# Optimization experiments

Measured on AMD Instinct MI355X. Metric: run time of the kernel, lower is better.

Reference implementation:

```python
import jax, jax.numpy as jnp
import numpy as np

B, N, D, H = 4, 2048, 1024, 16
HD = D // H


def setup_inputs() -> dict:
    key = jax.random.key(0)
    ks = jax.random.split(key, 9)
    s = 1.0 / np.sqrt(D)
    return {
        "x": jax.random.normal(ks[0], (B, N, D), jnp.float32),
        "Wq": jax.random.normal(ks[1], (D, D), jnp.float32) * s,
        "bq": jnp.zeros((D,), jnp.float32),
        "Wk": jax.random.normal(ks[2], (D, D), jnp.float32) * s,
        "bk": jnp.zeros((D,), jnp.float32),
        "Wv": jax.random.normal(ks[3], (D, D), jnp.float32) * s,
        "bv": jnp.zeros((D,), jnp.float32),
        "Wo": jax.random.normal(ks[4], (D, D), jnp.float32) * s,
        "bo": jnp.zeros((D,), jnp.float32),
    }


def reference(x, Wq, bq, Wk, bk, Wv, bv, Wo, bo):
    Bx, Nx, Dx = x.shape
    q = x @ Wq + bq  # [B,N,D]
    k = x @ Wk + bk
    v = x @ Wv + bv
    # split heads -> [B,H,N,hd]
    q = q.reshape(Bx, Nx, H, HD).transpose(0, 2, 1, 3)
    k = k.reshape(Bx, Nx, H, HD).transpose(0, 2, 1, 3)
    v = v.reshape(Bx, Nx, H, HD).transpose(0, 2, 1, 3)
    q = q / jnp.sqrt(jnp.asarray(HD, q.dtype))
    scores = jnp.einsum("bhqd,bhkd->bhqk", q, k)
    # causal mask: additive -1e9 strictly above diagonal (matches torch.triu diag=1)
    mask = jnp.triu(jnp.full((Nx, Nx), -1e9, dtype=scores.dtype), k=1)
    probs = jax.nn.softmax(scores + mask, axis=-1)
    out = jnp.einsum("bhqk,bhkd->bhqd", probs, v)  # [B,H,N,hd]
    out = out.transpose(0, 2, 1, 3).reshape(Bx, Nx, Dx)  # concat heads
    return out @ Wo + bo
```

## Files before the change

kernel.cpp:

```cpp
#include <hip/hip_runtime.h>
#include <hip/hip_bf16.h>


#define BB 4
#define NN 2048
#define DD 1024
#define HH 16
#define HD 64
#define MM (BB * NN)

typedef __bf16 bf16;
typedef __bf16 bf16x4 __attribute__((ext_vector_type(4)));
typedef __bf16 bf16x8 __attribute__((ext_vector_type(8)));
typedef float f32x4 __attribute__((ext_vector_type(4)));

__device__ __forceinline__ void async_copy16(bf16* lds, const bf16* g) {
    __builtin_amdgcn_global_load_lds(
        (const __attribute__((address_space(1))) void*)g,
        (__attribute__((address_space(3))) void*)lds, 16, 0, 0);
}

__global__ void convert_x(const float* __restrict__ x, bf16* __restrict__ xb) {
    int i = (blockIdx.x * 256 + threadIdx.x) * 4;
    float4 v = *(const float4*)&x[i];
    xb[i + 0] = (bf16)v.x;
    xb[i + 1] = (bf16)v.y;
    xb[i + 2] = (bf16)v.z;
    xb[i + 3] = (bf16)v.w;
}

__global__ void transpose_w4(const float* __restrict__ W0, const float* __restrict__ W1,
                             const float* __restrict__ W2, const float* __restrict__ W3,
                             bf16* __restrict__ Wt) {
    __shared__ float tile[32][33];
    const float* W = (blockIdx.z == 0) ? W0 : (blockIdx.z == 1) ? W1
                    : (blockIdx.z == 2) ? W2 : W3;
    bf16* out = Wt + (size_t)blockIdx.z * DD * DD;
    int tx = threadIdx.x, ty = threadIdx.y;
    int x0 = blockIdx.x * 32, y0 = blockIdx.y * 32;
#pragma unroll
    for (int i = 0; i < 32; i += 8)
        tile[ty + i][tx] = W[(size_t)(y0 + ty + i) * DD + x0 + tx];
    __syncthreads();
#pragma unroll
    for (int i = 0; i < 32; i += 8)
        out[(size_t)(x0 + ty + i) * DD + y0 + tx] = (bf16)tile[tx][ty + i];
}

template <int MODE>
__global__ __launch_bounds__(256) void gemm_bt(
    const bf16* __restrict__ A, const bf16* __restrict__ Wt,
    const float* __restrict__ b0, const float* __restrict__ b1,
    const float* __restrict__ b2, void* __restrict__ out0,
    void* __restrict__ out1, void* __restrict__ out2) {
    const int K = DD;
    __shared__ __align__(16) bf16 As[128 * 32];
    __shared__ __align__(16) bf16 Bs[128 * 32];
    __shared__ __align__(16) bf16 Cs[MODE == 0 ? 128 * 136 : 1];

    int m0 = blockIdx.x * 128;
    int n0 = blockIdx.y * 128;

    const bf16* Wz;
    const float* bias;
    void* out;
    float scale = 1.0f;
    int z = 0;
    if (MODE == 0) {
        z = blockIdx.z;
        Wz = Wt + (size_t)z * DD * DD;
        bias = (z == 0) ? b0 : ((z == 1) ? b1 : b2);
        out = (z == 0) ? out0 : ((z == 1) ? out1 : out2);
        if (z == 0) scale = 0.125f * 1.44269504f;
    } else {
        Wz = Wt; bias = b0; out = out0;
    }

    int tid = threadIdx.x;
    int w = tid >> 6, lane = tid & 63;
    int wm = w >> 1, wn = w & 1;
    int quad = lane >> 4, l16 = lane & 15;

    f32x4 acc[4][4];
#pragma unroll
    for (int i = 0; i < 4; i++)
#pragma unroll
        for (int j = 0; j < 4; j++) acc[i][j] = (f32x4){0.f, 0.f, 0.f, 0.f};

    for (int k0 = 0; k0 < K; k0 += 32) {
        __syncthreads();
#pragma unroll
        for (int j = 0; j < 2; j++) {
            int c = j * 256 + w * 64 + lane;
            int row = c >> 2, kk = (c & 3) * 8;
            async_copy16(&As[c * 8], &A[(size_t)(m0 + row) * K + k0 + kk]);
            async_copy16(&Bs[c * 8], &Wz[(size_t)(n0 + row) * K + k0 + kk]);
        }
        __syncthreads();

        bf16x8 af[4], bfm[4];
#pragma unroll
        for (int i = 0; i < 4; i++) {
            af[i] = *(const bf16x8*)&As[(wm * 64 + i * 16 + l16) * 32 + quad * 8];
            bfm[i] = *(const bf16x8*)&Bs[(wn * 64 + i * 16 + l16) * 32 + quad * 8];
        }
#pragma unroll
        for (int i = 0; i < 4; i++)
#pragma unroll
            for (int j = 0; j < 4; j++)
                acc[i][j] = __builtin_amdgcn_mfma_f32_16x16x32_bf16(
                    af[i], bfm[j], acc[i][j], 0, 0, 0);
    }

    if (MODE == 0) {
#pragma unroll
        for (int j = 0; j < 4; j++) {
            int nl = wn * 64 + j * 16 + l16;
            float bv = bias[n0 + nl];
#pragma unroll
            for (int i = 0; i < 4; i++) {
#pragma unroll
                for (int r = 0; r < 4; r++) {
                    int ml = wm * 64 + i * 16 + quad * 4 + r;
                    bf16 v = (bf16)((acc[i][j][r] + bv) * scale);
                    if (z == 2) Cs[nl * 136 + ml] = v;
                    else        Cs[ml * 136 + nl] = v;
                }
            }
        }
        __syncthreads();

        int bidx = m0 >> 11;
        int tok0 = m0 & (NN - 1);
        int hh0 = n0 >> 6;
        if (z != 2) {
#pragma unroll
            for (int hf = 0; hf < 2; hf++) {
                bf16* base = (bf16*)out + ((size_t)(bidx * HH + hh0 + hf) * NN + tok0) * HD;
#pragma unroll
                for (int k = 0; k < 4; k++) {
                    int f = k * 2048 + tid * 8;
                    int tok = f >> 6, hd = f & 63;
                    *(bf16x8*)&base[f] = *(const bf16x8*)&Cs[tok * 136 + hf * 64 + hd];
                }
            }
        } else {
#pragma unroll
            for (int hf = 0; hf < 2; hf++) {
#pragma unroll
                for (int k = 0; k < 4; k++) {
                    int hd = k * 16 + (tid >> 4);
                    int tk = (tid & 15) * 8;
                    bf16* dst = (bf16*)out +
                        ((size_t)(bidx * HH + hh0 + hf) * HD + hd) * NN + tok0 + tk;
                    *(bf16x8*)dst = *(const bf16x8*)&Cs[(hf * 64 + hd) * 136 + tk];
                }
            }
        }
    } else {
#pragma unroll
        for (int j = 0; j < 4; j++) {
            int n = n0 + wn * 64 + j * 16 + l16;
            float bv = bias[n];
#pragma unroll
            for (int i = 0; i < 4; i++) {
                int mrow = m0 + wm * 64 + i * 16 + quad * 4;
#pragma unroll
                for (int r = 0; r < 4; r++)
                    ((float*)out)[(size_t)(mrow + r) * DD + n] = acc[i][j][r] + bv;
            }
        }
    }
}

__global__ __launch_bounds__(512, 4) void flash_attn(
    const bf16* __restrict__ Q, const bf16* __restrict__ Kg,
    const bf16* __restrict__ Vt_g, bf16* __restrict__ Oc) {
    __shared__ __align__(16) bf16 Ks[128 * 72];
    __shared__ __align__(16) bf16 Vs[64 * 136];
    __shared__ __align__(16) bf16 Ps[128 * 136];

    int bh = blockIdx.x;
    int b = bh >> 4, h = bh & 15;
    int tid = threadIdx.x;
    int w = tid >> 6, lane = tid & 63;
    int quad = lane >> 4, l16 = lane & 15;

    const bf16* Qb = Q + (size_t)bh * NN * HD;
    const bf16* Kb = Kg + (size_t)bh * NN * HD;
    const bf16* Vtb = Vt_g + (size_t)bh * HD * NN;

    bf16x8 ones;
#pragma unroll
    for (int i = 0; i < 8; i++) ones[i] = (bf16)1.0f;

    int kr[2], kc[2], vd[2], vk[2];
#pragma unroll
    for (int j = 0; j < 2; j++) {
        int c = j * 512 + tid;
        kr[j] = c >> 3; kc[j] = (c & 7) * 8;
        vd[j] = c >> 4; vk[j] = (c & 15) * 8;
    }

    int psrow = (w * 16 + l16) * 136;

    for (int phase = 0; phase < 2; phase++) {
        int qi = (phase == 0) ? blockIdx.y : (15 - blockIdx.y);
        int q0 = qi * 128;
        int qrow = q0 + w * 16 + l16;

        bf16x8 qf[2];
#pragma unroll
        for (int ks = 0; ks < 2; ks++)
            qf[ks] = *(const bf16x8*)&Qb[(size_t)qrow * HD + ks * 32 + quad * 8];

        f32x4 l_sum = (f32x4){0.f, 0.f, 0.f, 0.f};
        f32x4 o_acc[4];
#pragma unroll
        for (int di = 0; di < 4; di++) o_acc[di] = (f32x4){0.f, 0.f, 0.f, 0.f};

        bf16x8 kreg[2], vreg[2];
#pragma unroll
        for (int j = 0; j < 2; j++) {
            kreg[j] = *(const bf16x8*)&Kb[(size_t)kr[j] * HD + kc[j]];
            vreg[j] = *(const bf16x8*)&Vtb[(size_t)vd[j] * NN + vk[j]];
        }

        for (int t = 0; t <= qi; t++) {
            __syncthreads();
#pragma unroll
            for (int j = 0; j < 2; j++) {
                *(bf16x8*)&Ks[kr[j] * 72 + kc[j]] = kreg[j];
                *(bf16x8*)&Vs[vd[j] * 136 + vk[j]] = vreg[j];
            }
            __syncthreads();

            if (t < qi) {
                int kvn = (t + 1) * 128;
#pragma unroll
                for (int j = 0; j < 2; j++) {
                    kreg[j] = *(const bf16x8*)&Kb[(size_t)(kvn + kr[j]) * HD + kc[j]];
                    vreg[j] = *(const bf16x8*)&Vtb[(size_t)vd[j] * NN + kvn + vk[j]];
                }
            }

            int kv0 = t * 128;
            bool diag = (t == qi);
#pragma unroll
            for (int ni = 0; ni < 8; ni++) {
                bf16x8 bk0 = *(const bf16x8*)&Ks[(ni * 16 + l16) * 72 + quad * 8];
                bf16x8 bk1 = *(const bf16x8*)&Ks[(ni * 16 + l16) * 72 + 32 + quad * 8];
                f32x4 s = (f32x4){0.f, 0.f, 0.f, 0.f};
                s = __builtin_amdgcn_mfma_f32_16x16x32_bf16(bk0, qf[0], s, 0, 0, 0);
                s = __builtin_amdgcn_mfma_f32_16x16x32_bf16(bk1, qf[1], s, 0, 0, 0);
                bf16x4 pv;
                if (diag) {
                    int kvb = kv0 + ni * 16 + quad * 4;
#pragma unroll
                    for (int r = 0; r < 4; r++)
                        pv[r] = (bf16)((kvb + r > qrow) ? 0.f : exp2f(s[r]));
                } else {
#pragma unroll
                    for (int r = 0; r < 4; r++) pv[r] = (bf16)exp2f(s[r]);
                }
                *(bf16x4*)&Ps[psrow + ni * 16 + quad * 4] = pv;
            }

#pragma unroll
            for (int ks = 0; ks < 4; ks++) {
                bf16x8 pf = *(const bf16x8*)&Ps[psrow + ks * 32 + quad * 8];
                l_sum = __builtin_amdgcn_mfma_f32_16x16x32_bf16(pf, ones, l_sum, 0, 0, 0);
#pragma unroll
                for (int di = 0; di < 4; di++) {
                    bf16x8 bv = *(const bf16x8*)&Vs[(di * 16 + l16) * 136 + ks * 32 + quad * 8];
                    o_acc[di] = __builtin_amdgcn_mfma_f32_16x16x32_bf16(pf, bv, o_acc[di], 0, 0, 0);
                }
            }
        }

#pragma unroll
        for (int r = 0; r < 4; r++) {
            float inv = 1.0f / l_sum[r];
            int tok = q0 + w * 16 + quad * 4 + r;
#pragma unroll
            for (int di = 0; di < 4; di++) {
                int d = h * 64 + di * 16 + l16;
                Oc[((size_t)(b * NN + tok)) * DD + d] = (bf16)(o_acc[di][r] * inv);
            }
        }
    }
}

extern "C" void kernel_launch(void* const* d_in, const int* in_sizes, int n_in,
                              void* d_out, int out_size, void* d_ws, size_t ws_size,
                              hipStream_t stream) {
    const float* x  = (const float*)d_in[0];
    const float* Wq = (const float*)d_in[1];
    const float* bq = (const float*)d_in[2];
    const float* Wk = (const float*)d_in[3];
    const float* bk = (const float*)d_in[4];
    const float* Wv = (const float*)d_in[5];
    const float* bv = (const float*)d_in[6];
    const float* Wo = (const float*)d_in[7];
    const float* bo = (const float*)d_in[8];

    const size_t need = (size_t)(8388608ull * 5 + 4194304ull) * sizeof(bf16);
    if (ws_size < need) return;

    bf16* ws = (bf16*)d_ws;
    bf16* xb = ws;
    bf16* wt = xb + (size_t)MM * DD;
    bf16* Qw = wt + 4ull * DD * DD;
    bf16* Kw = Qw + (size_t)MM * DD;
    bf16* Vw = Kw + (size_t)MM * DD;
    bf16* Aw = Vw + (size_t)MM * DD;

    convert_x<<<dim3(MM * DD / 1024), 256, 0, stream>>>(x, xb);

    transpose_w4<<<dim3(32, 32, 4), dim3(32, 8), 0, stream>>>(Wq, Wk, Wv, Wo, wt);

    gemm_bt<0><<<dim3(MM / 128, DD / 128, 3), 256, 0, stream>>>(
        xb, wt, bq, bk, bv, Qw, Kw, Vw);

    flash_attn<<<dim3(BB * HH, 8), 512, 0, stream>>>(Qw, Kw, Vw, Aw);

    gemm_bt<1><<<dim3(MM / 128, DD / 128, 1), 256, 0, stream>>>(
        Aw, wt + 3ull * DD * DD, bo, bo, bo, d_out, d_out, d_out);
}
```

Measured before the change: 256.6 us.

## Keep attention probabilities in registers via 16x16x16 MFMA and split query tiles

The P tile no longer round-trips through LDS. The QK^T accumulator layout is fed directly as the A operand of 16x16x16 bf16 MFMAs for both the row-sum and the PV product, which removes the Ps shared buffer and its writes and reads. Each block now handles a single query tile instead of a paired short and long tile, and the grid doubles to 16 tiles per head with a reordered tile schedule. Launch bounds are raised to 8 for higher occupancy. The cost is twice as many smaller MFMAs for PV, more blocks that each reload K/V, and less balanced per-block work.

```diff
diff --git a/kernel.cpp b/kernel.cpp
--- a/kernel.cpp
+++ b/kernel.cpp
@@ -13,6 +13,24 @@
 typedef __bf16 bf16x4 __attribute__((ext_vector_type(4)));
 typedef __bf16 bf16x8 __attribute__((ext_vector_type(8)));
 typedef float f32x4 __attribute__((ext_vector_type(4)));
+typedef short short4v __attribute__((ext_vector_type(4)));
+
+__device__ __forceinline__ f32x4 mfma16x16x16(short4v a, short4v b, f32x4 c) {
+#if defined(__HIP_DEVICE_COMPILE__)
+#if __has_builtin(__builtin_amdgcn_mfma_f32_16x16x16bf16_1k)
+    return __builtin_amdgcn_mfma_f32_16x16x16bf16_1k(a, b, c, 0, 0, 0);
+#else
+    f32x4 d;
+    asm("v_mfma_f32_16x16x16_bf16 %0, %1, %2, %3"
+        : "=&v"(d)
+        : "v"(a), "v"(b), "v"(c));
+    return d;
+#endif
+#else
+    (void)a; (void)b;
+    return c;
+#endif
+}
 
 __device__ __forceinline__ void async_copy16(bf16* lds, const bf16* g) {
     __builtin_amdgcn_global_load_lds(
@@ -173,12 +191,11 @@
     }
 }
 
-__global__ __launch_bounds__(512, 4) void flash_attn(
+__global__ __launch_bounds__(512, 8) void flash_attn(
     const bf16* __restrict__ Q, const bf16* __restrict__ Kg,
     const bf16* __restrict__ Vt_g, bf16* __restrict__ Oc) {
     __shared__ __align__(16) bf16 Ks[128 * 72];
     __shared__ __align__(16) bf16 Vs[64 * 136];
-    __shared__ __align__(16) bf16 Ps[128 * 136];
 
     int bh = blockIdx.x;
     int b = bh >> 4, h = bh & 15;
@@ -186,13 +203,16 @@
     int w = tid >> 6, lane = tid & 63;
     int quad = lane >> 4, l16 = lane & 15;
 
+    int y = blockIdx.y;
+    int ya = y & 3, bp = 3 - (y >> 2);
+    int qi = (bp < 2) ? (4 * bp + ya) : (4 * bp + 3 - ya);
+    int q0 = qi * 128;
+
     const bf16* Qb = Q + (size_t)bh * NN * HD;
     const bf16* Kb = Kg + (size_t)bh * NN * HD;
     const bf16* Vtb = Vt_g + (size_t)bh * HD * NN;
 
-    bf16x8 ones;
-#pragma unroll
-    for (int i = 0; i < 8; i++) ones[i] = (bf16)1.0f;
+    const short4v ones16 = {0x3F80, 0x3F80, 0x3F80, 0x3F80};
 
     int kr[2], kc[2], vd[2], vk[2];
 #pragma unroll
@@ -202,91 +222,80 @@
         vd[j] = c >> 4; vk[j] = (c & 15) * 8;
     }
 
-    int psrow = (w * 16 + l16) * 136;
-
-    for (int phase = 0; phase < 2; phase++) {
-        int qi = (phase == 0) ? blockIdx.y : (15 - blockIdx.y);
-        int q0 = qi * 128;
-        int qrow = q0 + w * 16 + l16;
-
-        bf16x8 qf[2];
-#pragma unroll
-        for (int ks = 0; ks < 2; ks++)
-            qf[ks] = *(const bf16x8*)&Qb[(size_t)qrow * HD + ks * 32 + quad * 8];
-
-        f32x4 l_sum = (f32x4){0.f, 0.f, 0.f, 0.f};
-        f32x4 o_acc[4];
-#pragma unroll
-        for (int di = 0; di < 4; di++) o_acc[di] = (f32x4){0.f, 0.f, 0.f, 0.f};
-
-        bf16x8 kreg[2], vreg[2];
+    int qrow = q0 + w * 16 + l16;
+
+    bf16x8 qf[2];
+#pragma unroll
+    for (int ks = 0; ks < 2; ks++)
+        qf[ks] = *(const bf16x8*)&Qb[(size_t)qrow * HD + ks * 32 + quad * 8];
+
+    f32x4 l_sum = (f32x4){0.f, 0.f, 0.f, 0.f};
+    f32x4 o_acc[4];
+#pragma unroll
+    for (int di = 0; di < 4; di++) o_acc[di] = (f32x4){0.f, 0.f, 0.f, 0.f};
+
+    bf16x8 kreg[2], vreg[2];
+#pragma unroll
+    for (int j = 0; j < 2; j++) {
+        kreg[j] = *(const bf16x8*)&Kb[(size_t)kr[j] * HD + kc[j]];
+        vreg[j] = *(const bf16x8*)&Vtb[(size_t)vd[j] * NN + vk[j]];
+    }
+
+    for (int t = 0; t <= qi; t++) {
+        __syncthreads();
 #pragma unroll
         for (int j = 0; j < 2; j++) {
-            kreg[j] = *(const bf16x8*)&Kb[(size_t)kr[j] * HD + kc[j]];
-            vreg[j] = *(const bf16x8*)&Vtb[(size_t)vd[j] * NN + vk[j]];
-        }
-
-        for (int t = 0; t <= qi; t++) {
-            __syncthreads();
+            *(bf16x8*)&Ks[kr[j] * 72 + kc[j]] = kreg[j];
+            *(bf16x8*)&Vs[vd[j] * 136 + vk[j]] = vreg[j];
+        }
+        __syncthreads();
+
+        if (t < qi) {
+            int kvn = (t + 1) * 128;
 #pragma unroll
             for (int j = 0; j < 2; j++) {
-                *(bf16x8*)&Ks[kr[j] * 72 + kc[j]] = kreg[j];
-                *(bf16x8*)&Vs[vd[j] * 136 + vk[j]] = vreg[j];
-            }
-            __syncthreads();
-
-            if (t < qi) {
-                int kvn = (t + 1) * 128;
-#pragma unroll
-                for (int j = 0; j < 2; j++) {
-                    kreg[j] = *(const bf16x8*)&Kb[(size_t)(kvn + kr[j]) * HD + kc[j]];
-                    vreg[j] = *(const bf16x8*)&Vtb[(size_t)vd[j] * NN + kvn + vk[j]];
-                }
-            }
-
-            int kv0 = t * 128;
-            bool diag = (t == qi);
-#pragma unroll
-            for (int ni = 0; ni < 8; ni++) {
-                bf16x8 bk0 = *(const bf16x8*)&Ks[(ni * 16 + l16) * 72 + quad * 8];
-                bf16x8 bk1 = *(const bf16x8*)&Ks[(ni * 16 + l16) * 72 + 32 + quad * 8];
-                f32x4 s = (f32x4){0.f, 0.f, 0.f, 0.f};
-                s = __builtin_amdgcn_mfma_f32_16x16x32_bf16(bk0, qf[0], s, 0, 0, 0);
-                s = __builtin_amdgcn_mfma_f32_16x16x32_bf16(bk1, qf[1], s, 0, 0, 0);
-                bf16x4 pv;
-                if (diag) {
-                    int kvb = kv0 + ni * 16 + quad * 4;
-#pragma unroll
-                    for (int r = 0; r < 4; r++)
-                        pv[r] = (bf16)((kvb + r > qrow) ? 0.f : exp2f(s[r]));
-                } else {
-#pragma unroll
-                    for (int r = 0; r < 4; r++) pv[r] = (bf16)exp2f(s[r]);
-                }
-                *(bf16x4*)&Ps[psrow + ni * 16 + quad * 4] = pv;
-            }
-
-#pragma unroll
-            for (int ks = 0; ks < 4; ks++) {
-                bf16x8 pf = *(const bf16x8*)&Ps[psrow + ks * 32 + quad * 8];
-                l_sum = __builtin_amdgcn_mfma_f32_16x16x32_bf16(pf, ones, l_sum, 0, 0, 0);
-#pragma unroll
-                for (int di = 0; di < 4; di++) {
-                    bf16x8 bv = *(const bf16x8*)&Vs[(di * 16 + l16) * 136 + ks * 32 + quad * 8];
-                    o_acc[di] = __builtin_amdgcn_mfma_f32_16x16x32_bf16(pf, bv, o_acc[di], 0, 0, 0);
-                }
-            }
-        }
-
-#pragma unroll
-        for (int r = 0; r < 4; r++) {
-            float inv = 1.0f / l_sum[r];
-            int tok = q0 + w * 16 + quad * 4 + r;
+                kreg[j] = *(const bf16x8*)&Kb[(size_t)(kvn + kr[j]) * HD + kc[j]];
+                vreg[j] = *(const bf16x8*)&Vtb[(size_t)vd[j] * NN + kvn + vk[j]];
+            }
+        }
+
+        int kv0 = t * 128;
+        bool diag = (t == qi);
+#pragma unroll
+        for (int ni = 0; ni < 8; ni++) {
+            bf16x8 bk0 = *(const bf16x8*)&Ks[(ni * 16 + l16) * 72 + quad * 8];
+            bf16x8 bk1 = *(const bf16x8*)&Ks[(ni * 16 + l16) * 72 + 32 + quad * 8];
+            f32x4 s = (f32x4){0.f, 0.f, 0.f, 0.f};
+            s = __builtin_amdgcn_mfma_f32_16x16x32_bf16(bk0, qf[0], s, 0, 0, 0);
+            s = __builtin_amdgcn_mfma_f32_16x16x32_bf16(bk1, qf[1], s, 0, 0, 0);
+            bf16x4 pb;
+            if (diag) {
+                int kvb = kv0 + ni * 16 + quad * 4;
+#pragma unroll
+                for (int r = 0; r < 4; r++)
+                    pb[r] = (bf16)((kvb + r > qrow) ? 0.f : exp2f(s[r]));
+            } else {
+#pragma unroll
+                for (int r = 0; r < 4; r++) pb[r] = (bf16)exp2f(s[r]);
+            }
+            short4v pv = __builtin_bit_cast(short4v, pb);
+            l_sum = mfma16x16x16(pv, ones16, l_sum);
 #pragma unroll
             for (int di = 0; di < 4; di++) {
-                int d = h * 64 + di * 16 + l16;
-                Oc[((size_t)(b * NN + tok)) * DD + d] = (bf16)(o_acc[di][r] * inv);
-            }
+                short4v vb = *(const short4v*)&Vs[(di * 16 + l16) * 136 + ni * 16 + quad * 4];
+                o_acc[di] = mfma16x16x16(pv, vb, o_acc[di]);
+            }
+        }
+    }
+
+#pragma unroll
+    for (int r = 0; r < 4; r++) {
+        float inv = 1.0f / l_sum[r];
+        int tok = q0 + w * 16 + quad * 4 + r;
+#pragma unroll
+        for (int di = 0; di < 4; di++) {
+            int d = h * 64 + di * 16 + l16;
+            Oc[((size_t)(b * NN + tok)) * DD + d] = (bf16)(o_acc[di][r] * inv);
         }
     }
 }
@@ -322,7 +331,7 @@
     gemm_bt<0><<<dim3(MM / 128, DD / 128, 3), 256, 0, stream>>>(
         xb, wt, bq, bk, bv, Qw, Kw, Vw);
 
-    flash_attn<<<dim3(BB * HH, 8), 512, 0, stream>>>(Qw, Kw, Vw, Aw);
+    flash_attn<<<dim3(BB * HH, 16), 512, 0, stream>>>(Qw, Kw, Vw, Aw);
 
     gemm_bt<1><<<dim3(MM / 128, DD / 128, 1), 256, 0, stream>>>(
         Aw, wt + 3ull * DD * DD, bo, bo, bo, d_out, d_out, d_out);
```

Measured after the change: 357.3 us. 39.2% more time.

## Keep attention probabilities in registers instead of staging through LDS

Applied to the files above, without the earlier changes.

The attention kernel no longer writes exp'd scores to a shared-memory P buffer and reads them back. It computes two 16-wide score tiles per step and packs them directly into the MFMA A-fragment. To make this work it permutes the K index mapping and reads V as two 4-element halves. The GEMM kernel also aliases its A/B staging buffers with the output-staging buffer to cut shared memory, at the cost of an extra barrier. Both changes reduce LDS footprint and traffic, which may raise occupancy, but V reads become narrower 8-byte loads.

```diff
diff --git a/kernel.cpp b/kernel.cpp
--- a/kernel.cpp
+++ b/kernel.cpp
@@ -54,9 +54,10 @@
     const float* __restrict__ b2, void* __restrict__ out0,
     void* __restrict__ out1, void* __restrict__ out2) {
     const int K = DD;
-    __shared__ __align__(16) bf16 As[128 * 32];
-    __shared__ __align__(16) bf16 Bs[128 * 32];
-    __shared__ __align__(16) bf16 Cs[MODE == 0 ? 128 * 136 : 1];
+    __shared__ __align__(16) bf16 smem[MODE == 0 ? 128 * 136 : 128 * 64];
+    bf16* As = smem;
+    bf16* Bs = smem + 128 * 32;
+    bf16* Cs = smem;
 
     int m0 = blockIdx.x * 128;
     int n0 = blockIdx.y * 128;
@@ -113,6 +114,7 @@
     }
 
     if (MODE == 0) {
+        __syncthreads();
 #pragma unroll
         for (int j = 0; j < 4; j++) {
             int nl = wn * 64 + j * 16 + l16;
@@ -178,7 +180,6 @@
     const bf16* __restrict__ Vt_g, bf16* __restrict__ Oc) {
     __shared__ __align__(16) bf16 Ks[128 * 72];
     __shared__ __align__(16) bf16 Vs[64 * 136];
-    __shared__ __align__(16) bf16 Ps[128 * 136];
 
     int bh = blockIdx.x;
     int b = bh >> 4, h = bh & 15;
@@ -190,9 +191,9 @@
     const bf16* Kb = Kg + (size_t)bh * NN * HD;
     const bf16* Vtb = Vt_g + (size_t)bh * HD * NN;
 
-    bf16x8 ones;
-#pragma unroll
-    for (int i = 0; i < 8; i++) ones[i] = (bf16)1.0f;
+    bf16x8 ones8;
+#pragma unroll
+    for (int i = 0; i < 8; i++) ones8[i] = (bf16)1.0f;
 
     int kr[2], kc[2], vd[2], vk[2];
 #pragma unroll
@@ -202,8 +203,6 @@
         vd[j] = c >> 4; vk[j] = (c & 15) * 8;
     }
 
-    int psrow = (w * 16 + l16) * 136;
-
     for (int phase = 0; phase < 2; phase++) {
         int qi = (phase == 0) ? blockIdx.y : (15 - blockIdx.y);
         int q0 = qi * 128;
@@ -247,33 +246,43 @@
             int kv0 = t * 128;
             bool diag = (t == qi);
 #pragma unroll
-            for (int ni = 0; ni < 8; ni++) {
-                bf16x8 bk0 = *(const bf16x8*)&Ks[(ni * 16 + l16) * 72 + quad * 8];
-                bf16x8 bk1 = *(const bf16x8*)&Ks[(ni * 16 + l16) * 72 + 32 + quad * 8];
-                f32x4 s = (f32x4){0.f, 0.f, 0.f, 0.f};
-                s = __builtin_amdgcn_mfma_f32_16x16x32_bf16(bk0, qf[0], s, 0, 0, 0);
-                s = __builtin_amdgcn_mfma_f32_16x16x32_bf16(bk1, qf[1], s, 0, 0, 0);
-                bf16x4 pv;
+            for (int mi = 0; mi < 4; mi++) {
+                int ba = 2 * mi, bb = 2 * mi + 1;
+                bf16x8 ka0 = *(const bf16x8*)&Ks[(ba * 16 + l16) * 72 + quad * 8];
+                bf16x8 ka1 = *(const bf16x8*)&Ks[(ba * 16 + l16) * 72 + 32 + quad * 8];
+                bf16x8 kb0 = *(const bf16x8*)&Ks[(bb * 16 + l16) * 72 + quad * 8];
+                bf16x8 kb1 = *(const bf16x8*)&Ks[(bb * 16 + l16) * 72 + 32 + quad * 8];
+                f32x4 sa = (f32x4){0.f, 0.f, 0.f, 0.f};
+                f32x4 sb = (f32x4){0.f, 0.f, 0.f, 0.f};
+                sa = __builtin_amdgcn_mfma_f32_16x16x32_bf16(ka0, qf[0], sa, 0, 0, 0);
+                sa = __builtin_amdgcn_mfma_f32_16x16x32_bf16(ka1, qf[1], sa, 0, 0, 0);
+                sb = __builtin_amdgcn_mfma_f32_16x16x32_bf16(kb0, qf[0], sb, 0, 0, 0);
+                sb = __builtin_amdgcn_mfma_f32_16x16x32_bf16(kb1, qf[1], sb, 0, 0, 0);
+                bf16x4 pa4, pb4;
                 if (diag) {
-                    int kvb = kv0 + ni * 16 + quad * 4;
-#pragma unroll
-                    for (int r = 0; r < 4; r++)
-                        pv[r] = (bf16)((kvb + r > qrow) ? 0.f : exp2f(s[r]));
+                    int kva = kv0 + ba * 16 + quad * 4;
+                    int kvb = kv0 + bb * 16 + quad * 4;
+#pragma unroll
+                    for (int r = 0; r < 4; r++) {
+                        pa4[r] = (bf16)((kva + r > qrow) ? 0.f : exp2f(sa[r]));
+                        pb4[r] = (bf16)((kvb + r > qrow) ? 0.f : exp2f(sb[r]));
+                    }
                 } else {
 #pragma unroll
-                    for (int r = 0; r < 4; r++) pv[r] = (bf16)exp2f(s[r]);
-                }
-                *(bf16x4*)&Ps[psrow + ni * 16 + quad * 4] = pv;
-            }
-
-#pragma unroll
-            for (int ks = 0; ks < 4; ks++) {
-                bf16x8 pf = *(const bf16x8*)&Ps[psrow + ks * 32 + quad * 8];
-                l_sum = __builtin_amdgcn_mfma_f32_16x16x32_bf16(pf, ones, l_sum, 0, 0, 0);
+                    for (int r = 0; r < 4; r++) {
+                        pa4[r] = (bf16)exp2f(sa[r]);
+                        pb4[r] = (bf16)exp2f(sb[r]);
+                    }
+                }
+                bf16x8 pfrag = __builtin_shufflevector(pa4, pb4, 0, 1, 2, 3, 4, 5, 6, 7);
+                l_sum = __builtin_amdgcn_mfma_f32_16x16x32_bf16(pfrag, ones8, l_sum, 0, 0, 0);
 #pragma unroll
                 for (int di = 0; di < 4; di++) {
-                    bf16x8 bv = *(const bf16x8*)&Vs[(di * 16 + l16) * 136 + ks * 32 + quad * 8];
-                    o_acc[di] = __builtin_amdgcn_mfma_f32_16x16x32_bf16(pf, bv, o_acc[di], 0, 0, 0);
+                    const bf16* vrow = &Vs[(di * 16 + l16) * 136 + mi * 32 + quad * 4];
+                    bf16x4 vlo = *(const bf16x4*)(vrow);
+                    bf16x4 vhi = *(const bf16x4*)(vrow + 16);
+                    bf16x8 vfrag = __builtin_shufflevector(vlo, vhi, 0, 1, 2, 3, 4, 5, 6, 7);
+                    o_acc[di] = __builtin_amdgcn_mfma_f32_16x16x32_bf16(pfrag, vfrag, o_acc[di], 0, 0, 0);
                 }
             }
         }
```

After: 265.7 us. 1.04x slower.
